# Kernel optimization log

Hardware: AMD Instinct MI355X
Metric: run time of the kernel (lower is better)

Reference implementation:

```python
import jax, jax.numpy as jnp
import numpy as np

D = 2048      # d_model
H = 32        # n_heads
DS = 64       # d_state = d_model // n_heads
K = 4         # conv kernel size (hardcoded in module)
EPS = 1e-6


def setup_inputs() -> dict:
    key = jax.random.key(0)
    ks = jax.random.split(key, 8)
    B, L = 2, 4096
    s = lambda k, shp, sc: jax.random.normal(k, shp, dtype=jnp.float32) * sc
    return {
        "x": s(ks[0], (B, L, D), 1.0),
        "state": jnp.zeros((B, H, DS), jnp.float32),
        "norm_w": jnp.ones((D,), jnp.float32),
        "conv_w": s(ks[1], (D, K), 0.5),          # depthwise conv weight [d_model, K]
        "conv_b": s(ks[2], (D,), 0.1),
        "pp_w": s(ks[3], (D, 3 * H * DS), 0.02),  # param_proj (stored [in, out])
        "pp_b": jnp.zeros((3 * H * DS,), jnp.float32),
        "gp_w": s(ks[4], (D, D), 0.02),           # gate_proj
        "gp_b": jnp.zeros((D,), jnp.float32),
        "op_w": s(ks[5], (D, D), 0.02),           # out_proj
        "op_b": jnp.zeros((D,), jnp.float32),
    }


def reference(x, state, norm_w, conv_w, conv_b, pp_w, pp_b, gp_w, gp_b, op_w, op_b):
    B, L, Dm = x.shape
    # RMSNorm
    rms = jnp.sqrt(jnp.mean(x * x, axis=-1, keepdims=True) + EPS)
    xn = norm_w * x / rms
    # causal depthwise conv1d + SiLU (pad left K-1, valid cross-correlation)
    xp = jnp.pad(xn, ((0, 0), (K - 1, 0), (0, 0)))
    xc = conv_b + sum(xp[:, k:k + L, :] * conv_w[:, k] for k in range(K))
    xc = jax.nn.silu(xc)
    gate = jax.nn.sigmoid(xc @ gp_w + gp_b)                  # [B, L, D]
    p = (xn @ pp_w + pp_b).reshape(B, L, H, 3, DS)
    delta = jax.nn.sigmoid(p[..., 0, :])                     # [B, L, H, DS]
    Bm, Cm = p[..., 1, :], p[..., 2, :]
    # sequential recurrence h_t = delta_t * h_{t-1} + B_t, time-major scan
    dt = jnp.moveaxis(delta, 1, 0)                           # [L, B, H, DS]
    Bt = jnp.moveaxis(Bm, 1, 0)
    def step(h, db):
        d, b = db
        h = d * h + b
        return h, h
    h_last, hs = jax.lax.scan(step, state, (dt, Bt))         # hs: [L, B, H, DS]
    ssm = (jnp.moveaxis(Cm, 1, 0) * hs).reshape(L, B, Dm)
    ssm = jnp.moveaxis(ssm, 0, 1)                            # [B, L, D]
    mixed = gate * ssm + (1.0 - gate) * xn
    y = mixed @ op_w + op_b + x
    return y, h_last
```

## Files before the change

kernel.cpp:

```cpp
#include <hip/hip_runtime.h>
#include <math.h>

#define BB   2
#define LL   4096
#define DD   2048
#define HH   32
#define DSS  64
#define MM   (BB * LL)
#define N3   (3 * HH * DSS)
#define NCH  64
#define CLN  64
#define EPSF 1e-6f
#define GP_NB (DD / 128)
#define PP_NB (N3 / 128)
#define TR_NBX 320
#define TR_NBY (DD / 32)

typedef unsigned short bf16;
typedef __attribute__((ext_vector_type(8))) short bf16x8;
typedef __attribute__((ext_vector_type(4))) float f32x4;

__device__ __forceinline__ float bf2f(bf16 u) {
    union { unsigned int i; float f; } v;
    v.i = ((unsigned int)u) << 16;
    return v.f;
}
__device__ __forceinline__ bf16 f2bf(float f) {
    union { float f; unsigned int u; } v;
    v.f = f;
    unsigned int r = (v.u >> 16) & 1u;
    return (bf16)((v.u + 0x7fffu + r) >> 16);
}
__device__ __forceinline__ float sigmoidf_(float v) {
    return 1.0f / (1.0f + __expf(-v));
}
__device__ __forceinline__ void gload16(const void* g, void* l) {
    __builtin_amdgcn_global_load_lds(
        (const __attribute__((address_space(1))) void*)g,
        (__attribute__((address_space(3))) void*)l, 16, 0, 0);
}

__global__ __launch_bounds__(256) void rms_transpose(const float* __restrict__ x,
                                                     const float* __restrict__ w,
                                                     bf16* __restrict__ xn,
                                                     const float* __restrict__ gp_w,
                                                     const float* __restrict__ op_w,
                                                     const float* __restrict__ pp_w,
                                                     bf16* __restrict__ gp_wT,
                                                     bf16* __restrict__ op_wT,
                                                     bf16* __restrict__ pp_wT) {
    __shared__ float sh[32 * 33];
    int t = threadIdx.x;
    if (blockIdx.x < MM) {
        int row = blockIdx.x;
        const float4* x4 = (const float4*)(x + (size_t)row * DD);
        ushort4* o4 = (ushort4*)(xn + (size_t)row * DD);
        const float4* w4 = (const float4*)w;
        float4 v0 = x4[t], v1 = x4[t + 256];
        float ss = v0.x * v0.x + v0.y * v0.y + v0.z * v0.z + v0.w * v0.w +
                   v1.x * v1.x + v1.y * v1.y + v1.z * v1.z + v1.w * v1.w;
#pragma unroll
        for (int off = 32; off >= 1; off >>= 1) ss += __shfl_down(ss, off, 64);
        if ((t & 63) == 0) sh[t >> 6] = ss;
        __syncthreads();
        float tot = sh[0] + sh[1] + sh[2] + sh[3];
        float inv = 1.0f / sqrtf(tot * (1.0f / DD) + EPSF);
        float4 wa = w4[t], wb = w4[t + 256];
        ushort4 r0, r1;
        r0.x = f2bf(v0.x * inv * wa.x); r0.y = f2bf(v0.y * inv * wa.y);
        r0.z = f2bf(v0.z * inv * wa.z); r0.w = f2bf(v0.w * inv * wa.w);
        r1.x = f2bf(v1.x * inv * wb.x); r1.y = f2bf(v1.y * inv * wb.y);
        r1.z = f2bf(v1.z * inv * wb.z); r1.w = f2bf(v1.w * inv * wb.w);
        o4[t] = r0; o4[t + 256] = r1;
    } else {
        int id = blockIdx.x - MM;
        int bx = id % TR_NBX;
        int k0 = (id / TR_NBX) << 5;
        const float* W; bf16* WT; int Ndim;
        if (bx < 64)       { W = gp_w; WT = gp_wT; Ndim = DD; }
        else if (bx < 128) { W = op_w; WT = op_wT; Ndim = DD; bx -= 64; }
        else               { W = pp_w; WT = pp_wT; Ndim = N3; bx -= 128; }
        int n0 = bx << 5;
        float (*tl)[33] = (float (*)[33])sh;
        int tx = t & 31, ty = t >> 5;
#pragma unroll
        for (int i = 0; i < 32; i += 8)
            tl[ty + i][tx] = W[(size_t)(k0 + ty + i) * Ndim + n0 + tx];
        __syncthreads();
        int tx2 = t & 15, ty2 = t >> 4;
#pragma unroll
        for (int i = 0; i < 32; i += 16) {
            int n = ty2 + i;
            ushort2 v = { f2bf(tl[tx2 * 2][n]), f2bf(tl[tx2 * 2 + 1][n]) };
            *(ushort2*)&WT[(size_t)(n0 + n) * DD + k0 + tx2 * 2] = v;
        }
    }
}

#define CONV_LC 16
__global__ __launch_bounds__(256) void conv_silu_kernel(const bf16* __restrict__ xn,
                                                        const float* __restrict__ cw,
                                                        const float* __restrict__ cb,
                                                        bf16* __restrict__ xc) {
    int b = blockIdx.z;
    int l0 = blockIdx.x * CONV_LC;
    int d0 = blockIdx.y * 1024 + threadIdx.x * 4;
    float4 w[4];
    float bias[4];
#pragma unroll
    for (int j = 0; j < 4; ++j) {
        w[j] = ((const float4*)cw)[d0 + j];
        bias[j] = cb[d0 + j];
    }
    float win[3][4];
#pragma unroll
    for (int k = 0; k < 3; ++k) {
        int l = l0 - 3 + k;
        if (l >= 0) {
            ushort4 v = *(const ushort4*)&xn[((size_t)b * LL + l) * DD + d0];
            win[k][0] = bf2f(v.x); win[k][1] = bf2f(v.y);
            win[k][2] = bf2f(v.z); win[k][3] = bf2f(v.w);
        } else {
            win[k][0] = win[k][1] = win[k][2] = win[k][3] = 0.0f;
        }
    }
    size_t off = ((size_t)b * LL + l0) * DD + d0;
#pragma unroll 4
    for (int i = 0; i < CONV_LC; ++i) {
        ushort4 v = *(const ushort4*)&xn[off];
        float cur[4] = {bf2f(v.x), bf2f(v.y), bf2f(v.z), bf2f(v.w)};
        ushort4 o;
#pragma unroll
        for (int j = 0; j < 4; ++j) {
            float acc = bias[j] + win[0][j] * w[j].x + win[1][j] * w[j].y +
                        win[2][j] * w[j].z + cur[j] * w[j].w;
            float s = acc * sigmoidf_(acc);
            ((unsigned short*)&o)[j] = f2bf(s);
        }
        *(ushort4*)&xc[off] = o;
#pragma unroll
        for (int j = 0; j < 4; ++j) {
            win[0][j] = win[1][j]; win[1][j] = win[2][j]; win[2][j] = cur[j];
        }
        off += DD;
    }
}

template <int EPI, typename OutT>
__device__ __forceinline__ void gemm_tile(const bf16* __restrict__ A,
                                          const bf16* __restrict__ Bt,
                                          const float* __restrict__ bias,
                                          const float* __restrict__ add,
                                          OutT* __restrict__ out,
                                          int Ndim, int m0, int n0,
                                          bf16* As, bf16* Bs) {
    const int tid  = threadIdx.x;
    const int wave = tid >> 6;
    const int lane = tid & 63;
    const int sr = lane >> 3;
    const int gcol = ((lane & 7) ^ sr) << 3;
    const bf16* gA[4];
    const bf16* gB[4];
    bf16* lA[4];
    bf16* lB[4];
#pragma unroll
    for (int p = 0; p < 4; ++p) {
        int c = wave * 4 + p;
        gA[p] = A  + (size_t)(m0 + c * 8 + sr) * DD + gcol;
        gB[p] = Bt + (size_t)(n0 + c * 8 + sr) * DD + gcol;
        lA[p] = As + c * 512 + lane * 8;
        lB[p] = Bs + c * 512 + lane * 8;
    }
    const int wm = (wave >> 1) << 6;
    const int wn = (wave & 1) << 6;
    const int fr = lane & 15;
    const int kg = lane >> 4;
    const int f7 = fr & 7;

    f32x4 acc[4][4] = {};
    for (int k0 = 0; k0 < DD; k0 += 64) {
        __syncthreads();
#pragma unroll
        for (int p = 0; p < 4; ++p) {
            gload16(gA[p] + k0, lA[p]);
            gload16(gB[p] + k0, lB[p]);
        }
        __syncthreads();
#pragma unroll
        for (int ks = 0; ks < 2; ++ks) {
            bf16x8 af[4], bf_[4];
#pragma unroll
            for (int i = 0; i < 4; ++i) {
                int gq = (((ks << 2) | kg) ^ f7) << 3;
                af[i]  = *(const bf16x8*)&As[(wm + i * 16 + fr) * 64 + gq];
                bf_[i] = *(const bf16x8*)&Bs[(wn + i * 16 + fr) * 64 + gq];
            }
#pragma unroll
            for (int i = 0; i < 4; ++i)
#pragma unroll
                for (int j = 0; j < 4; ++j)
                    acc[i][j] = __builtin_amdgcn_mfma_f32_16x16x32_bf16(
                        af[i], bf_[j], acc[i][j], 0, 0, 0);
        }
    }
    const int baseRow = m0 + wm + kg * 4;
    const int baseCol = n0 + wn + fr;
#pragma unroll
    for (int i = 0; i < 4; ++i) {
#pragma unroll
        for (int r = 0; r < 4; ++r) {
            int m = baseRow + i * 16 + r;
            size_t rowoff = (size_t)m * Ndim + baseCol;
#pragma unroll
            for (int j = 0; j < 4; ++j) {
                float v = acc[i][j][r] + bias[baseCol + j * 16];
                if (EPI == 1) v = sigmoidf_(v);
                if (EPI == 2) v += add[rowoff + j * 16];
                if constexpr (sizeof(OutT) == 4)
                    ((float*)out)[rowoff + j * 16] = v;
                else
                    ((bf16*)out)[rowoff + j * 16] = f2bf(v);
            }
        }
    }
}

__global__ __launch_bounds__(256) void gemm_gateproj(const bf16* __restrict__ xc,
                                                     const bf16* __restrict__ gp_wT,
                                                     const float* __restrict__ gp_b,
                                                     bf16* __restrict__ gate,
                                                     const bf16* __restrict__ xn,
                                                     const bf16* __restrict__ pp_wT,
                                                     const float* __restrict__ pp_b,
                                                     bf16* __restrict__ p) {
    __shared__ __align__(16) bf16 As[128 * 64];
    __shared__ __align__(16) bf16 Bs[128 * 64];
    const int m0 = blockIdx.y << 7;
    if (blockIdx.x < GP_NB) {
        gemm_tile<1, bf16>(xc, gp_wT, gp_b, nullptr, gate, DD,
                           m0, blockIdx.x << 7, As, Bs);
    } else {
        gemm_tile<0, bf16>(xn, pp_wT, pp_b, nullptr, p, N3,
                           m0, (blockIdx.x - GP_NB) << 7, As, Bs);
    }
}

__global__ __launch_bounds__(256) void gemm_out(const bf16* __restrict__ mixed,
                                                const bf16* __restrict__ op_wT,
                                                const float* __restrict__ op_b,
                                                const float* __restrict__ x,
                                                float* __restrict__ y) {
    __shared__ __align__(16) bf16 As[128 * 64];
    __shared__ __align__(16) bf16 Bs[128 * 64];
    gemm_tile<2, float>(mixed, op_wT, op_b, x, y, DD,
                        blockIdx.y << 7, blockIdx.x << 7, As, Bs);
}


__global__ __launch_bounds__(256) void scan_phase1(const bf16* __restrict__ p,
                                                   float* __restrict__ cA,
                                                   float* __restrict__ cB) {
    int c = blockIdx.x, b = blockIdx.z, s = threadIdx.x & 63;
    int h = blockIdx.y * 4 + (threadIdx.x >> 6);
    size_t base = ((size_t)(b * LL + c * CLN)) * N3 + h * (3 * DSS) + s;
    float a = 1.0f, bb = 0.0f;
#pragma unroll 8
    for (int i = 0; i < CLN; ++i) {
        float d = sigmoidf_(bf2f(p[base]));
        float Bv = bf2f(p[base + DSS]);
        a *= d;
        bb = d * bb + Bv;
        base += N3;
    }
    int idx = ((b * HH + h) * NCH + c) * DSS + s;
    cA[idx] = a;
    cB[idx] = bb;
}

__global__ __launch_bounds__(256) void scan_phase3(const bf16* __restrict__ p,
                                                   const float* __restrict__ cA,
                                                   const float* __restrict__ cB,
                                                   const float* __restrict__ state,
                                                   const bf16* __restrict__ gate,
                                                   const bf16* __restrict__ xn,
                                                   bf16* __restrict__ mixed,
                                                   float* __restrict__ hlast) {
    int c = blockIdx.x, b = blockIdx.z, s = threadIdx.x & 63;
    int h = blockIdx.y * 4 + (threadIdx.x >> 6);
    float hp = state[(b * HH + h) * DSS + s];
    int cbase = ((b * HH + h) * NCH) * DSS + s;
    for (int cc = 0; cc < c; ++cc)
        hp = cA[cbase + cc * DSS] * hp + cB[cbase + cc * DSS];
    size_t prow = ((size_t)(b * LL + c * CLN)) * N3 + h * (3 * DSS) + s;
    size_t grow = ((size_t)(b * LL + c * CLN)) * DD + h * DSS + s;
#pragma unroll 4
    for (int i = 0; i < CLN; ++i) {
        float d = sigmoidf_(bf2f(p[prow]));
        float Bv = bf2f(p[prow + DSS]);
        float Cv = bf2f(p[prow + 2 * DSS]);
        hp = d * hp + Bv;
        float ssm = Cv * hp;
        float g = bf2f(gate[grow]);
        float xv = bf2f(xn[grow]);
        mixed[grow] = f2bf(g * ssm + (1.0f - g) * xv);
        prow += N3;
        grow += DD;
    }
    if (c == NCH - 1) hlast[(b * HH + h) * DSS + s] = hp;
}

extern "C" void kernel_launch(void* const* d_in, const int* in_sizes, int n_in,
                              void* d_out, int out_size, void* d_ws, size_t ws_size,
                              hipStream_t stream) {
    const float* x      = (const float*)d_in[0];
    const float* state  = (const float*)d_in[1];
    const float* norm_w = (const float*)d_in[2];
    const float* conv_w = (const float*)d_in[3];
    const float* conv_b = (const float*)d_in[4];
    const float* pp_w   = (const float*)d_in[5];
    const float* pp_b   = (const float*)d_in[6];
    const float* gp_w   = (const float*)d_in[7];
    const float* gp_b   = (const float*)d_in[8];
    const float* op_w   = (const float*)d_in[9];
    const float* op_b   = (const float*)d_in[10];

    float* y     = (float*)d_out;
    float* hlast = y + (size_t)MM * DD;

    const size_t BHND = (size_t)BB * HH * NCH * DSS;
    char* ws = (char*)d_ws;
    bf16* xn    = (bf16*)ws;
    bf16* xcbuf = xn + (size_t)MM * DD;
    bf16* p     = xcbuf + (size_t)MM * DD;
    float* cA   = (float*)(p + (size_t)MM * N3);
    float* cB   = cA + BHND;
    bf16* gp_wT = (bf16*)(cB + BHND);
    bf16* op_wT = gp_wT + (size_t)DD * DD;
    bf16* gate  = (bf16*)y;
    bf16* pp_wT = gate + (size_t)MM * DD;
    bf16* mixed = xcbuf;

    rms_transpose<<<MM + TR_NBX * TR_NBY, 256, 0, stream>>>(
        x, norm_w, xn, gp_w, op_w, pp_w, gp_wT, op_wT, pp_wT);
    conv_silu_kernel<<<dim3(LL / CONV_LC, DD / 1024, BB), 256, 0, stream>>>(
        xn, conv_w, conv_b, xcbuf);
    gemm_gateproj<<<dim3(GP_NB + PP_NB, MM / 128), 256, 0, stream>>>(
        xcbuf, gp_wT, gp_b, gate, xn, pp_wT, pp_b, p);
    scan_phase1<<<dim3(NCH, HH / 4, BB), 256, 0, stream>>>(p, cA, cB);
    scan_phase3<<<dim3(NCH, HH / 4, BB), 256, 0, stream>>>(
        p, cA, cB, state, gate, xn, mixed, hlast);
    gemm_out<<<dim3(GP_NB, MM / 128), 256, 0, stream>>>(mixed, op_wT, op_b, x, y);
}
```

Before: 670.5 us.

## Rewrite GEMMs as 256x256 double-buffered pipelined tiles with XCD-aware block remap

Replaces the 128x128 single-buffered GEMM tile with a 256x256 tile computed by 8 waves. Global-to-LDS loads for the next K step are double-buffered and interleaved with four MFMA quadrants, using explicit barriers, waitcnt and setprio. Block indices are remapped so neighbouring tiles land on the same XCD for better L2 reuse. The goal is to hide load latency and raise MFMA utilisation. The cost is 128 KB of LDS per block, higher register pressure and fragile hand-written synchronisation.

```diff
diff --git a/kernel.cpp b/kernel.cpp
--- a/kernel.cpp
+++ b/kernel.cpp
@@ -11,10 +11,11 @@
 #define NCH  64
 #define CLN  64
 #define EPSF 1e-6f
-#define GP_NB (DD / 128)
-#define PP_NB (N3 / 128)
 #define TR_NBX 320
 #define TR_NBY (DD / 32)
+#define NT   (DD / 64)
+#define GT_NB (DD / 256)
+#define PJ_NB (N3 / 256)
 
 typedef unsigned short bf16;
 typedef __attribute__((ext_vector_type(8))) short bf16x8;
@@ -39,6 +40,10 @@
         (const __attribute__((address_space(1))) void*)g,
         (__attribute__((address_space(3))) void*)l, 16, 0, 0);
 }
+
+#define SBAR()  asm volatile("s_barrier" ::: "memory")
+#define LGKM0() asm volatile("s_waitcnt lgkmcnt(0)" ::: "memory")
+#define VMC(n)  asm volatile("s_waitcnt vmcnt(" #n ")" ::: "memory")
 
 __global__ __launch_bounds__(256) void rms_transpose(const float* __restrict__ x,
                                                      const float* __restrict__ w,
@@ -147,113 +152,194 @@
 }
 
 template <int EPI, typename OutT>
-__device__ __forceinline__ void gemm_tile(const bf16* __restrict__ A,
-                                          const bf16* __restrict__ Bt,
-                                          const float* __restrict__ bias,
-                                          const float* __restrict__ add,
-                                          OutT* __restrict__ out,
-                                          int Ndim, int m0, int n0,
-                                          bf16* As, bf16* Bs) {
+__device__ __forceinline__ void gemm_tile256(const bf16* __restrict__ A,
+                                             const bf16* __restrict__ Bt,
+                                             const float* __restrict__ bias,
+                                             const float* __restrict__ add,
+                                             OutT* __restrict__ out,
+                                             int Ndim, int m0, int n0,
+                                             bf16* lds) {
     const int tid  = threadIdx.x;
     const int wave = tid >> 6;
     const int lane = tid & 63;
-    const int sr = lane >> 3;
+    const int sr   = lane >> 3;
     const int gcol = ((lane & 7) ^ sr) << 3;
-    const bf16* gA[4];
-    const bf16* gB[4];
-    bf16* lA[4];
-    bf16* lB[4];
-#pragma unroll
-    for (int p = 0; p < 4; ++p) {
-        int c = wave * 4 + p;
-        gA[p] = A  + (size_t)(m0 + c * 8 + sr) * DD + gcol;
-        gB[p] = Bt + (size_t)(n0 + c * 8 + sr) * DD + gcol;
-        lA[p] = As + c * 512 + lane * 8;
-        lB[p] = Bs + c * 512 + lane * 8;
-    }
-    const int wm = (wave >> 1) << 6;
-    const int wn = (wave & 1) << 6;
+    const bf16* gA = A  + (size_t)(m0 + wave * 16 + sr) * DD + gcol;
+    const bf16* gB = Bt + (size_t)(n0 + wave * 16 + sr) * DD + gcol;
+    const int ldst = wave * 1024 + lane * 8;
+
     const int fr = lane & 15;
     const int kg = lane >> 4;
     const int f7 = fr & 7;
-
-    f32x4 acc[4][4] = {};
-    for (int k0 = 0; k0 < DD; k0 += 64) {
-        __syncthreads();
-#pragma unroll
-        for (int p = 0; p < 4; ++p) {
-            gload16(gA[p] + k0, lA[p]);
-            gload16(gB[p] + k0, lB[p]);
-        }
-        __syncthreads();
-#pragma unroll
-        for (int ks = 0; ks < 2; ++ks) {
-            bf16x8 af[4], bf_[4];
-#pragma unroll
-            for (int i = 0; i < 4; ++i) {
-                int gq = (((ks << 2) | kg) ^ f7) << 3;
-                af[i]  = *(const bf16x8*)&As[(wm + i * 16 + fr) * 64 + gq];
-                bf_[i] = *(const bf16x8*)&Bs[(wn + i * 16 + fr) * 64 + gq];
-            }
+    const int wm = (wave >> 2) << 6;
+    const int wn = (wave & 3) << 5;
+
+    auto STAGE = [&](int bufsel, int half, int tau) {
+        const bf16* src = (half < 2 ? gA : gB) +
+                          (size_t)((half & 1) << 7) * DD + tau * 64;
+        bf16* dst = lds + bufsel * 32768 + half * 8192 + ldst;
+        gload16(src, dst);
+        gload16(src + 8 * DD, dst + 512);
+    };
+
+    f32x4 acc[8][4] = {};
+    bf16x8 af[4][2], b0[2][2], b1[2][2];
+
+    STAGE(0, 0, 0); STAGE(0, 3, 0); STAGE(0, 1, 0); STAGE(0, 2, 0);
+    STAGE(1, 0, 1); STAGE(1, 3, 1);
+    VMC(4);
+    SBAR();
+
+#pragma unroll 2
+    for (int tau = 0; tau < NT; ++tau) {
+        bf16* Ls = lds + (tau & 1) * 32768;
+#pragma unroll
+        for (int i = 0; i < 4; ++i)
+#pragma unroll
+            for (int ks = 0; ks < 2; ++ks)
+                af[i][ks] = *(const bf16x8*)&Ls[(wm + i * 16 + fr) * 64 +
+                                               ((((ks << 2) | kg) ^ f7) << 3)];
+#pragma unroll
+        for (int j = 0; j < 2; ++j)
+#pragma unroll
+            for (int ks = 0; ks < 2; ++ks)
+                b0[j][ks] = *(const bf16x8*)&Ls[2 * 8192 + (wn + j * 16 + fr) * 64 +
+                                               ((((ks << 2) | kg) ^ f7) << 3)];
+        if (tau + 1 < NT) STAGE((tau + 1) & 1, 1, tau + 1);
+        SBAR(); LGKM0();
+        __builtin_amdgcn_sched_barrier(0);
+        __builtin_amdgcn_s_setprio(1);
+#pragma unroll
+        for (int ks = 0; ks < 2; ++ks)
 #pragma unroll
             for (int i = 0; i < 4; ++i)
 #pragma unroll
-                for (int j = 0; j < 4; ++j)
+                for (int j = 0; j < 2; ++j)
                     acc[i][j] = __builtin_amdgcn_mfma_f32_16x16x32_bf16(
-                        af[i], bf_[j], acc[i][j], 0, 0, 0);
-        }
-    }
-    const int baseRow = m0 + wm + kg * 4;
+                        af[i][ks], b0[j][ks], acc[i][j], 0, 0, 0);
+        __builtin_amdgcn_sched_barrier(0);
+        __builtin_amdgcn_s_setprio(0);
+        SBAR();
+#pragma unroll
+        for (int j = 0; j < 2; ++j)
+#pragma unroll
+            for (int ks = 0; ks < 2; ++ks)
+                b1[j][ks] = *(const bf16x8*)&Ls[3 * 8192 + (wn + j * 16 + fr) * 64 +
+                                               ((((ks << 2) | kg) ^ f7) << 3)];
+        if (tau + 1 < NT) STAGE((tau + 1) & 1, 2, tau + 1);
+        SBAR(); LGKM0();
+        __builtin_amdgcn_sched_barrier(0);
+        __builtin_amdgcn_s_setprio(1);
+#pragma unroll
+        for (int ks = 0; ks < 2; ++ks)
+#pragma unroll
+            for (int i = 0; i < 4; ++i)
+#pragma unroll
+                for (int j = 0; j < 2; ++j)
+                    acc[i][2 + j] = __builtin_amdgcn_mfma_f32_16x16x32_bf16(
+                        af[i][ks], b1[j][ks], acc[i][2 + j], 0, 0, 0);
+        __builtin_amdgcn_sched_barrier(0);
+        __builtin_amdgcn_s_setprio(0);
+        SBAR();
+#pragma unroll
+        for (int i = 0; i < 4; ++i)
+#pragma unroll
+            for (int ks = 0; ks < 2; ++ks)
+                af[i][ks] = *(const bf16x8*)&Ls[8192 + (wm + i * 16 + fr) * 64 +
+                                               ((((ks << 2) | kg) ^ f7) << 3)];
+        if (tau + 2 < NT) STAGE(tau & 1, 0, tau + 2);
+        SBAR(); LGKM0();
+        __builtin_amdgcn_sched_barrier(0);
+        __builtin_amdgcn_s_setprio(1);
+#pragma unroll
+        for (int ks = 0; ks < 2; ++ks)
+#pragma unroll
+            for (int i = 0; i < 4; ++i)
+#pragma unroll
+                for (int j = 0; j < 2; ++j)
+                    acc[4 + i][2 + j] = __builtin_amdgcn_mfma_f32_16x16x32_bf16(
+                        af[i][ks], b1[j][ks], acc[4 + i][2 + j], 0, 0, 0);
+        __builtin_amdgcn_sched_barrier(0);
+        __builtin_amdgcn_s_setprio(0);
+        SBAR();
+        if (tau + 2 < NT) STAGE(tau & 1, 3, tau + 2);
+        if (tau < NT - 2) { VMC(4); } else { VMC(0); }
+        SBAR(); LGKM0();
+        __builtin_amdgcn_sched_barrier(0);
+        __builtin_amdgcn_s_setprio(1);
+#pragma unroll
+        for (int ks = 0; ks < 2; ++ks)
+#pragma unroll
+            for (int i = 0; i < 4; ++i)
+#pragma unroll
+                for (int j = 0; j < 2; ++j)
+                    acc[4 + i][j] = __builtin_amdgcn_mfma_f32_16x16x32_bf16(
+                        af[i][ks], b0[j][ks], acc[4 + i][j], 0, 0, 0);
+        __builtin_amdgcn_sched_barrier(0);
+        __builtin_amdgcn_s_setprio(0);
+        SBAR();
+    }
+
+    const int baseRow = m0 + wm + (kg << 2);
     const int baseCol = n0 + wn + fr;
-#pragma unroll
-    for (int i = 0; i < 4; ++i) {
+    float bia[4];
+#pragma unroll
+    for (int nf = 0; nf < 4; ++nf)
+        bia[nf] = bias[baseCol + (nf >> 1) * 128 + (nf & 1) * 16];
+#pragma unroll
+    for (int mf = 0; mf < 8; ++mf) {
 #pragma unroll
         for (int r = 0; r < 4; ++r) {
-            int m = baseRow + i * 16 + r;
+            int m = baseRow + (mf >> 2) * 128 + (mf & 3) * 16 + r;
             size_t rowoff = (size_t)m * Ndim + baseCol;
 #pragma unroll
-            for (int j = 0; j < 4; ++j) {
-                float v = acc[i][j][r] + bias[baseCol + j * 16];
+            for (int nf = 0; nf < 4; ++nf) {
+                size_t off = rowoff + (nf >> 1) * 128 + (nf & 1) * 16;
+                float v = acc[mf][nf][r] + bia[nf];
                 if (EPI == 1) v = sigmoidf_(v);
-                if (EPI == 2) v += add[rowoff + j * 16];
+                if (EPI == 2) v += add[off];
                 if constexpr (sizeof(OutT) == 4)
-                    ((float*)out)[rowoff + j * 16] = v;
+                    ((float*)out)[off] = v;
                 else
-                    ((bf16*)out)[rowoff + j * 16] = f2bf(v);
+                    ((bf16*)out)[off] = f2bf(v);
             }
         }
     }
 }
 
-__global__ __launch_bounds__(256) void gemm_gateproj(const bf16* __restrict__ xc,
-                                                     const bf16* __restrict__ gp_wT,
-                                                     const float* __restrict__ gp_b,
-                                                     bf16* __restrict__ gate,
-                                                     const bf16* __restrict__ xn,
-                                                     const bf16* __restrict__ pp_wT,
-                                                     const float* __restrict__ pp_b,
-                                                     bf16* __restrict__ p) {
-    __shared__ __align__(16) bf16 As[128 * 64];
-    __shared__ __align__(16) bf16 Bs[128 * 64];
-    const int m0 = blockIdx.y << 7;
-    if (blockIdx.x < GP_NB) {
-        gemm_tile<1, bf16>(xc, gp_wT, gp_b, nullptr, gate, DD,
-                           m0, blockIdx.x << 7, As, Bs);
-    } else {
-        gemm_tile<0, bf16>(xn, pp_wT, pp_b, nullptr, p, N3,
-                           m0, (blockIdx.x - GP_NB) << 7, As, Bs);
-    }
-}
-
-__global__ __launch_bounds__(256) void gemm_out(const bf16* __restrict__ mixed,
-                                                const bf16* __restrict__ op_wT,
-                                                const float* __restrict__ op_b,
-                                                const float* __restrict__ x,
-                                                float* __restrict__ y) {
-    __shared__ __align__(16) bf16 As[128 * 64];
-    __shared__ __align__(16) bf16 Bs[128 * 64];
-    gemm_tile<2, float>(mixed, op_wT, op_b, x, y, DD,
-                        blockIdx.y << 7, blockIdx.x << 7, As, Bs);
+__global__ __launch_bounds__(512, 2) void gemm_gateproj(const bf16* __restrict__ xc,
+                                                        const bf16* __restrict__ gp_wT,
+                                                        const float* __restrict__ gp_b,
+                                                        bf16* __restrict__ gate,
+                                                        const bf16* __restrict__ xn,
+                                                        const bf16* __restrict__ pp_wT,
+                                                        const float* __restrict__ pp_b,
+                                                        bf16* __restrict__ p) {
+    __shared__ __align__(16) bf16 lds[2 * 4 * 8192];
+    int fid = blockIdx.x;
+    int f = (fid & 7) * 128 + (fid >> 3);
+    int by = f >> 5;
+    int bx = f & 31;
+    int m0 = by << 8;
+    if (bx < GT_NB)
+        gemm_tile256<1, bf16>(xc, gp_wT, gp_b, nullptr, gate, DD,
+                              m0, bx << 8, lds);
+    else
+        gemm_tile256<0, bf16>(xn, pp_wT, pp_b, nullptr, p, N3,
+                              m0, (bx - GT_NB) << 8, lds);
+}
+
+__global__ __launch_bounds__(512, 2) void gemm_out(const bf16* __restrict__ mixed,
+                                                   const bf16* __restrict__ op_wT,
+                                                   const float* __restrict__ op_b,
+                                                   const float* __restrict__ x,
+                                                   float* __restrict__ y) {
+    __shared__ __align__(16) bf16 lds[2 * 4 * 8192];
+    int fid = blockIdx.x;
+    int f = (fid & 7) * 32 + (fid >> 3);
+    int m0 = (f >> 3) << 8;
+    int n0 = (f & 7) << 8;
+    gemm_tile256<2, float>(mixed, op_wT, op_b, x, y, DD, m0, n0, lds);
 }
 
 
@@ -344,10 +430,10 @@
         x, norm_w, xn, gp_w, op_w, pp_w, gp_wT, op_wT, pp_wT);
     conv_silu_kernel<<<dim3(LL / CONV_LC, DD / 1024, BB), 256, 0, stream>>>(
         xn, conv_w, conv_b, xcbuf);
-    gemm_gateproj<<<dim3(GP_NB + PP_NB, MM / 128), 256, 0, stream>>>(
+    gemm_gateproj<<<(GT_NB + PJ_NB) * (MM / 256), 512, 0, stream>>>(
         xcbuf, gp_wT, gp_b, gate, xn, pp_wT, pp_b, p);
     scan_phase1<<<dim3(NCH, HH / 4, BB), 256, 0, stream>>>(p, cA, cB);
     scan_phase3<<<dim3(NCH, HH / 4, BB), 256, 0, stream>>>(
         p, cA, cB, state, gate, xn, mixed, hlast);
-    gemm_out<<<dim3(GP_NB, MM / 128), 256, 0, stream>>>(mixed, op_wT, op_b, x, y);
-}
+    gemm_out<<<MM / 256 * (DD / 256), 512, 0, stream>>>(mixed, op_wT, op_b, x, y);
+}
```

Result: faster. 578.6 us (-13.7%).
